# Kernel tuning notes

Hardware: AMD Instinct MI355X
Metric: run time of the kernel (lower is better)

## Reference

```python
import jax, jax.numpy as jnp
import numpy as np

KSIZE = 3
BJORCK_ITERS = 20
POWER_ITERS = 10


def _power_iteration_sigma(A, u):
    # A: [K, n, n], u: [K, n, 1] -> leading singular value per matrix, [K]
    for _ in range(POWER_ITERS):
        v = jnp.swapaxes(A, -1, -2) @ u
        v = v / jnp.linalg.norm(v, axis=-2, keepdims=True)
        u = A @ v
        u = u / jnp.linalg.norm(u, axis=-2, keepdims=True)
    s = (jnp.swapaxes(u, -1, -2) @ A @ v)[..., 0, 0]
    return s


def _bjorck(w, u):
    # power-iteration scaling is done under no_grad in torch -> stop_gradient
    s = jax.lax.stop_gradient(_power_iteration_sigma(jax.lax.stop_gradient(w), u))
    w = w / s[:, None, None]
    for _ in range(BJORCK_ITERS):
        wtw = jnp.swapaxes(w, -1, -2) @ w
        w = 1.5 * w - 0.5 * (w @ wtw)  # beta = 0.5, first order
    return w


def _block_orth(p1, p2):
    # -> [2, 2, n, n]
    n = p1.shape[0]
    I = jnp.eye(n, dtype=p1.dtype)
    return jnp.stack([
        jnp.stack([p1 @ p2, p1 @ (I - p2)]),
        jnp.stack([(I - p1) @ p2, (I - p1) @ (I - p2)]),
    ])


def _matrix_conv(m1, m2):
    # m1: [k,k,n,n], m2: [l,l,n,n] -> [k+l-1, k+l-1, n, n]
    k, l = m1.shape[0], m2.shape[0]
    size = k + l - 1
    rows = []
    for i in range(size):
        row = []
        for j in range(size):
            acc = 0.0
            for i1 in range(min(k, i + 1)):
                for j1 in range(min(k, j + 1)):
                    if i - i1 < l and j - j1 < l:
                        acc = acc + m1[i1, j1] @ m2[i - i1, j - j1]
            row.append(acc)
        rows.append(jnp.stack(row))
    return jnp.stack(rows)


def _bcop_weight(param_matrices, init_u):
    K, C, _ = param_matrices.shape  # K = 2*(KSIZE-1)+1, C = max_channels
    ortho = _bjorck(param_matrices, init_u)
    H = ortho[0]  # cin == cout == C, full slice
    half = C // 2
    mask = jnp.concatenate(
        [jnp.ones((K - 1, 1, half), ortho.dtype), jnp.zeros((K - 1, 1, C - half), ortho.dtype)],
        axis=-1)
    PQ = ortho[1:] * mask
    PQ = PQ @ jnp.swapaxes(PQ, -1, -2)  # symmetric projections [K-1, C, C]
    p = _block_orth(PQ[0], PQ[1])
    for t in range(1, KSIZE - 1):
        p = _matrix_conv(p, _block_orth(PQ[2 * t], PQ[2 * t + 1]))
    p = jnp.einsum('ab,ijbc->ijac', H, p)  # H @ p[i,j]
    # dict_to_tensor(...).permute(3, 2, 1, 0): [k, k, r, c] -> [c, r, j, i]
    return jnp.transpose(p, (3, 2, 1, 0))  # [C_out, C_in, KSIZE, KSIZE]


def setup_inputs() -> dict:
    key = jax.random.key(0)
    k1, k2, k3, k4 = jax.random.split(key, 4)
    C = 256
    num_kernels = 2 * (KSIZE - 1) + 1
    x = jax.random.normal(k1, (32, C, 64, 64), dtype=jnp.float32)
    param_matrices = jax.random.normal(k2, (num_kernels, C, C), dtype=jnp.float32) / np.sqrt(C)
    init_u = jax.random.normal(k3, (num_kernels, C, 1), dtype=jnp.float32)
    bias = jax.random.uniform(k4, (C,), dtype=jnp.float32, minval=-1.0 / np.sqrt(C), maxval=1.0 / np.sqrt(C))
    return {"x": x, "param_matrices": param_matrices, "init_u": init_u, "bias": bias}


def reference(x, param_matrices, init_u, bias):
    weight = _bcop_weight(param_matrices, init_u)
    # cyclic (circular) padding by k//2 on each side, odd kernel
    pad = KSIZE // 2
    xp = jnp.pad(x, ((0, 0), (0, 0), (pad, pad), (pad, pad)), mode='wrap')
    out = jax.lax.conv_general_dilated(
        xp, weight, window_strides=(1, 1), padding='VALID',
        dimension_numbers=('NCHW', 'OIHW', 'NCHW'))
    return out + bias[None, :, None, None]
```

## Files before the change

kernel.cpp:

```cpp
#include <hip/hip_runtime.h>
#include <stdint.h>

typedef unsigned short u16;
typedef unsigned short u16x4 __attribute__((ext_vector_type(4)));
typedef short bf16x8 __attribute__((ext_vector_type(8)));
typedef float f32x4 __attribute__((ext_vector_type(4)));

#define CDIM 256
#define MSZ 65536

constexpr size_t O_XB   = 0;
constexpr size_t O_AT   = 67108864;
constexpr size_t O_PQH  = 67108864;
constexpr size_t O_PQL  = O_PQH + 524288;
constexpr size_t O_SVAL = 68419584;
constexpr size_t O_W0   = 68419840;
constexpr size_t O_W1   = 71041280;
constexpr size_t O_PH   = 71041280;
constexpr size_t O_PL   = O_PH + 524288;
constexpr size_t O_QTH  = O_PL + 524288;
constexpr size_t O_QTL  = O_QTH + 524288;
constexpr size_t O_TH   = 73662720;
constexpr size_t O_TL   = O_TH + 655360;
constexpr size_t O_RTH  = 74973440;
constexpr size_t O_RTL  = O_RTH + 1179648;
constexpr size_t O_WBQ  = O_RTL + 1179648;

__device__ __forceinline__ u16 f2bf(float f) {
  union { float f; uint32_t u; } a; a.f = f;
  uint32_t u = a.u;
  uint32_t r = u + 0x7FFFu + ((u >> 16) & 1u);
  return (u16)(r >> 16);
}
__device__ __forceinline__ float bf2f(u16 u) {
  union { uint32_t u; float f; } a; a.u = ((uint32_t)u) << 16; return a.f;
}
__device__ __forceinline__ void split_st(u16* hi, u16* lo, float v) {
  u16 h = f2bf(v);
  *hi = h;
  *lo = f2bf(v - bf2f(h));
}
__device__ __forceinline__ void gl16(const void* g, void* l) {
  __builtin_amdgcn_global_load_lds(
      (const __attribute__((address_space(1))) void*)g,
      (__attribute__((address_space(3))) void*)l, 16, 0, 0);
}

__global__ void convert_k(const float* __restrict__ x, u16* __restrict__ xb) {
  __shared__ float t[32][33];
  int b = blockIdx.x;
  int ctile = b & 7, wtile = (b >> 3) & 1, h = (b >> 4) & 63, n = b >> 10;
  int c0 = ctile * 32, w0 = wtile * 32;
  int tid = threadIdx.x;
  for (int p = 0; p < 4; p++) {
    int e = tid + p * 256; int cc = e >> 5, ww = e & 31;
    t[cc][ww] = x[(((size_t)n * 256 + c0 + cc) * 64 + h) * 64 + w0 + ww];
  }
  __syncthreads();
  {
    int ww = tid >> 3, c4 = (tid & 7) * 4;
    u16x4 v;
    #pragma unroll
    for (int j = 0; j < 4; ++j) v[j] = f2bf(t[c4 + j][ww]);
    *(u16x4*)&xb[(((size_t)n * 64 + h) * 64 + w0 + ww) * 256 + c0 + c4] = v;
  }
}

__global__ void wtwA_k(const float* __restrict__ W, float* __restrict__ T) {
  int m = blockIdx.y;
  int i0 = (blockIdx.x >> 3) * 32, j0 = (blockIdx.x & 7) * 32;
  const float* A = W + (size_t)m * MSZ;
  __shared__ float As[32][33], Bs[32][33];
  int tid = threadIdx.x, tx = tid & 15, ty = tid >> 4;
  float a00 = 0, a01 = 0, a10 = 0, a11 = 0;
  for (int kc = 0; kc < CDIM; kc += 32) {
    __syncthreads();
    for (int p = 0; p < 4; p++) {
      int e = tid + p * 256; int kk = e >> 5, cc = e & 31;
      As[kk][cc] = A[(kc + kk) * CDIM + i0 + cc];
      Bs[kk][cc] = A[(kc + kk) * CDIM + j0 + cc];
    }
    __syncthreads();
    #pragma unroll
    for (int kk = 0; kk < 32; kk++) {
      float av0 = As[kk][ty], av1 = As[kk][ty + 16];
      float bv0 = Bs[kk][tx], bv1 = Bs[kk][tx + 16];
      a00 += av0 * bv0; a01 += av0 * bv1; a10 += av1 * bv0; a11 += av1 * bv1;
    }
  }
  float* Tm = T + (size_t)m * MSZ;
  Tm[(i0 + ty) * CDIM + j0 + tx] = a00;
  Tm[(i0 + ty) * CDIM + j0 + tx + 16] = a01;
  Tm[(i0 + ty + 16) * CDIM + j0 + tx] = a10;
  Tm[(i0 + ty + 16) * CDIM + j0 + tx + 16] = a11;
}

__global__ __launch_bounds__(1024) void powerB_k(const float* __restrict__ A,
                                                 const float* __restrict__ B,
                                                 const float* __restrict__ u0,
                                                 float* __restrict__ sval) {
  int m = blockIdx.x;
  int tid = threadIdx.x;
  int t = tid & 255, s = tid >> 8;
  __shared__ float v[256], part[4][257];
  const float* Am = A + (size_t)m * MSZ;
  const float* Bm = B + (size_t)m * MSZ;
  float a = 0.f;
  #pragma unroll 16
  for (int i = 0; i < 64; ++i) a += Am[(s * 64 + i) * 256 + t] * u0[m * 256 + s * 64 + i];
  part[s][t] = a;
  __syncthreads();
  if (s == 0) v[t] = part[0][t] + part[1][t] + part[2][t] + part[3][t];
  __syncthreads();
  for (int it = 0; it < 9; ++it) {
    float b = 0.f;
    #pragma unroll 16
    for (int j = 0; j < 64; ++j) b += Bm[(s * 64 + j) * 256 + t] * v[s * 64 + j];
    part[s][t] = b;
    __syncthreads();
    if (s == 0) v[t] = part[0][t] + part[1][t] + part[2][t] + part[3][t];
    __syncthreads();
  }
  float b = 0.f;
  #pragma unroll 16
  for (int j = 0; j < 64; ++j) b += Bm[(s * 64 + j) * 256 + t] * v[s * 64 + j];
  part[s][t] = b;
  __syncthreads();
  if (s == 0) {
    float w = part[0][t] + part[1][t] + part[2][t] + part[3][t];
    float vv = v[t];
    float d1 = vv * w, d2 = vv * vv;
    for (int off = 32; off; off >>= 1) {
      d1 += __shfl_down(d1, off);
      d2 += __shfl_down(d2, off);
    }
    if ((t & 63) == 0) { part[1][t >> 6] = d1; part[2][t >> 6] = d2; }
  }
  __syncthreads();
  if (tid == 0) {
    float num = part[1][0] + part[1][1] + part[1][2] + part[1][3];
    float den = part[2][0] + part[2][1] + part[2][2] + part[2][3];
    sval[m] = sqrtf(num / den);
  }
}

__global__ void scaleT_k(const float* __restrict__ param, const float* __restrict__ sval,
                         u16* __restrict__ Wh, u16* __restrict__ Wl,
                         u16* __restrict__ Wth, u16* __restrict__ Wtl) {
  __shared__ float tl[32][33];
  int m = blockIdx.y;
  int i0 = (blockIdx.x >> 3) * 32, j0 = (blockIdx.x & 7) * 32;
  int tid = threadIdx.x;
  float inv = 1.0f / sval[m];
  const float* Am = param + (size_t)m * MSZ;
  size_t mo = (size_t)m * MSZ;
  for (int p = 0; p < 4; ++p) {
    int e = tid + p * 256; int ii = e >> 5, jj = e & 31;
    float v = Am[(i0 + ii) * 256 + j0 + jj] * inv;
    tl[ii][jj] = v;
    size_t idx = mo + (size_t)(i0 + ii) * 256 + j0 + jj;
    split_st(&Wh[idx], &Wl[idx], v);
  }
  __syncthreads();
  for (int p = 0; p < 4; ++p) {
    int e = tid + p * 256; int jj = e >> 5, ii = e & 31;
    float v = tl[ii][jj];
    size_t idxT = mo + (size_t)(j0 + jj) * 256 + i0 + ii;
    split_st(&Wth[idxT], &Wtl[idxT], v);
  }
}

__device__ __forceinline__ void gemm32_acc(
    const u16* __restrict__ Ah, const u16* __restrict__ Al, int i0,
    const u16* __restrict__ Bh, const u16* __restrict__ Bl, int j0,
    int K, f32x4* acc, char* smem, int tid)
{
  int lane = tid & 63, wave = tid >> 6;
  int qm = wave >> 1, qn = wave & 1;
  int ra = qm * 16 + (lane & 15);
  int rb = qn * 16 + (lane & 15);
  int kb = (lane >> 4) * 16;
  for (int kc = 0; kc < K; kc += 128) {
    __syncthreads();
    #pragma unroll
    for (int p = 0; p < 8; ++p) {
      int e = tid + p * 256;
      int bufi = e >> 9;
      int r = (e >> 4) & 31;
      int cb = (e & 15) * 16;
      const u16* srcm = (bufi == 0) ? Ah : (bufi == 1) ? Al : (bufi == 2) ? Bh : Bl;
      int r0 = (bufi < 2) ? i0 : j0;
      const char* src = (const char*)srcm + ((size_t)(r0 + r) * 256 + kc) * 2 + cb;
      *(uint4*)(smem + bufi * 8192 + r * 256 + (cb ^ ((r & 7) << 4))) = *(const uint4*)src;
    }
    __syncthreads();
    #pragma unroll
    for (int ks = 0; ks < 4; ++ks) {
      int kbyte = ks * 64 + kb;
      int oa = ra * 256 + (kbyte ^ ((ra & 7) << 4));
      int ob = rb * 256 + (kbyte ^ ((rb & 7) << 4));
      bf16x8 ah = *(const bf16x8*)(smem + oa);
      bf16x8 al = *(const bf16x8*)(smem + 8192 + oa);
      bf16x8 bh = *(const bf16x8*)(smem + 16384 + ob);
      bf16x8 bl = *(const bf16x8*)(smem + 24576 + ob);
      *acc = __builtin_amdgcn_mfma_f32_16x16x32_bf16(ah, bh, *acc, 0, 0, 0);
      *acc = __builtin_amdgcn_mfma_f32_16x16x32_bf16(ah, bl, *acc, 0, 0, 0);
      *acc = __builtin_amdgcn_mfma_f32_16x16x32_bf16(al, bh, *acc, 0, 0, 0);
    }
  }
}

#define GEMM_IDX \
  int tid = threadIdx.x; \
  int lane = tid & 63, wave = tid >> 6, qm = wave >> 1, qn = wave & 1; \
  int orow = qm * 16 + ((lane >> 4) << 2); \
  int ocol = qn * 16 + (lane & 15); \
  int i0 = (blockIdx.x >> 3) * 32, j0 = (blockIdx.x & 7) * 32; \
  __shared__ char smem[32768];

__global__ __launch_bounds__(256) void bjorck_t_k(
    const u16* __restrict__ Wth, const u16* __restrict__ Wtl,
    u16* __restrict__ Th, u16* __restrict__ Tl) {
  GEMM_IDX
  size_t mo = (size_t)blockIdx.y * MSZ;
  f32x4 acc = {};
  gemm32_acc(Wth + mo, Wtl + mo, i0, Wth + mo, Wtl + mo, j0, 256, &acc, smem, tid);
  #pragma unroll
  for (int v = 0; v < 4; ++v) {
    size_t idx = mo + (size_t)(i0 + orow + v) * 256 + (j0 + ocol);
    split_st(&Th[idx], &Tl[idx], acc[v]);
  }
}

__global__ __launch_bounds__(256) void bjorck_u_k(
    const u16* __restrict__ Wh, const u16* __restrict__ Wl,
    const u16* __restrict__ Th, const u16* __restrict__ Tl,
    u16* __restrict__ nWh, u16* __restrict__ nWl,
    u16* __restrict__ nWth, u16* __restrict__ nWtl) {
  GEMM_IDX
  size_t mo = (size_t)blockIdx.y * MSZ;
  f32x4 acc = {};
  gemm32_acc(Wh + mo, Wl + mo, i0, Th + mo, Tl + mo, j0, 256, &acc, smem, tid);
  #pragma unroll
  for (int v = 0; v < 4; ++v) {
    int r = i0 + orow + v, c = j0 + ocol;
    size_t idx = mo + (size_t)r * 256 + c;
    float wv = bf2f(Wh[idx]) + bf2f(Wl[idx]);
    float nv = 1.5f * wv - 0.5f * acc[v];
    split_st(&nWh[idx], &nWl[idx], nv);
    size_t idxT = mo + (size_t)c * 256 + r;
    split_st(&nWth[idxT], &nWtl[idxT], nv);
  }
}

__global__ __launch_bounds__(256) void pq_k(
    const u16* __restrict__ Wh, const u16* __restrict__ Wl,
    u16* __restrict__ PQh, u16* __restrict__ PQl) {
  GEMM_IDX
  int m4 = blockIdx.y;
  const u16* Oh = Wh + (size_t)(1 + m4) * MSZ;
  const u16* Ol = Wl + (size_t)(1 + m4) * MSZ;
  f32x4 acc = {};
  gemm32_acc(Oh, Ol, i0, Oh, Ol, j0, 128, &acc, smem, tid);
  #pragma unroll
  for (int v = 0; v < 4; ++v) {
    size_t idx = (size_t)m4 * MSZ + (size_t)(i0 + orow + v) * 256 + (j0 + ocol);
    split_st(&PQh[idx], &PQl[idx], acc[v]);
  }
}

__global__ __launch_bounds__(256) void c12b_k(
    const u16* __restrict__ PQh, const u16* __restrict__ PQl,
    u16* __restrict__ Ph, u16* __restrict__ Pl,
    u16* __restrict__ QTh, u16* __restrict__ QTl) {
  GEMM_IDX
  f32x4 a1 = {}, a2t = {};
  gemm32_acc(PQh, PQl, i0, PQh + MSZ, PQl + MSZ, j0, 256, &a1, smem, tid);
  gemm32_acc(PQh + 3 * MSZ, PQl + 3 * MSZ, i0, PQh + 2 * MSZ, PQl + 2 * MSZ, j0,
             256, &a2t, smem, tid);
  #pragma unroll
  for (int v = 0; v < 4; ++v) {
    int row = i0 + orow + v, col = j0 + ocol;
    size_t g = (size_t)row * 256 + col;
    float I = (row == col) ? 1.f : 0.f;
    float p0 = bf2f(PQh[g]) + bf2f(PQl[g]);
    float p1 = bf2f(PQh[MSZ + g]) + bf2f(PQl[MSZ + g]);
    float c1 = a1[v];
    split_st(&Ph[g],           &Pl[g],           c1);
    split_st(&Ph[MSZ + g],     &Pl[MSZ + g],     p0 - c1);
    split_st(&Ph[2*MSZ + g],   &Pl[2*MSZ + g],   p1 - c1);
    split_st(&Ph[3*MSZ + g],   &Pl[3*MSZ + g],   I - p0 - p1 + c1);
    float q0 = bf2f(PQh[2*MSZ + g]) + bf2f(PQl[2*MSZ + g]);
    float q1 = bf2f(PQh[3*MSZ + g]) + bf2f(PQl[3*MSZ + g]);
    float c2t = a2t[v];
    split_st(&QTh[g],          &QTl[g],          c2t);
    split_st(&QTh[MSZ + g],    &QTl[MSZ + g],    q0 - c2t);
    split_st(&QTh[2*MSZ + g],  &QTl[2*MSZ + g],  q1 - c2t);
    split_st(&QTh[3*MSZ + g],  &QTl[3*MSZ + g],  I - q0 - q1 + c2t);
  }
}

__global__ __launch_bounds__(256) void mconv_k(
    const u16* __restrict__ Ph, const u16* __restrict__ Pl,
    const u16* __restrict__ QTh, const u16* __restrict__ QTl,
    u16* __restrict__ RTh, u16* __restrict__ RTl) {
  GEMM_IDX
  int ij = blockIdx.y;
  const int toff[10] = {0, 1, 3, 4, 6, 10, 12, 13, 15, 16};
  const int tp[16] = {0, 0, 1, 1, 0, 2, 0, 1, 2, 3, 1, 3, 2, 2, 3, 3};
  const int tq[16] = {0, 1, 0, 1, 2, 0, 3, 2, 1, 0, 3, 1, 2, 3, 2, 3};
  f32x4 acc = {};
  for (int t = toff[ij]; t < toff[ij + 1]; ++t) {
    gemm32_acc(Ph + (size_t)tp[t] * MSZ, Pl + (size_t)tp[t] * MSZ, i0,
               QTh + (size_t)tq[t] * MSZ, QTl + (size_t)tq[t] * MSZ, j0, 256, &acc, smem, tid);
  }
  #pragma unroll
  for (int v = 0; v < 4; ++v) {
    int r = i0 + orow + v, c = j0 + ocol;
    size_t idxT = (size_t)ij * MSZ + (size_t)c * 256 + r;
    split_st(&RTh[idxT], &RTl[idxT], acc[v]);
  }
}

__global__ __launch_bounds__(256) void final_k(
    const u16* __restrict__ Hh, const u16* __restrict__ Hl,
    const u16* __restrict__ RTh, const u16* __restrict__ RTl,
    u16* __restrict__ WBQ) {
  GEMM_IDX
  int ij = blockIdx.y;
  f32x4 acc = {};
  gemm32_acc(Hh, Hl, i0, RTh + (size_t)ij * MSZ, RTl + (size_t)ij * MSZ, j0,
             256, &acc, smem, tid);
  #pragma unroll
  for (int v = 0; v < 4; ++v) {
    int r = i0 + orow + v, c = j0 + ocol;
    int ct = r >> 6, ks = (r >> 5) & 1, jj = (r >> 3) & 3, e = r & 7;
    int s = jj ^ (c & 3);
    int g = ct * 18 + ij * 2 + ks;
    WBQ[(size_t)g * 8192 + (size_t)(c * 4 + s) * 8 + e] = f2bf(acc[v]);
  }
}

__global__ __launch_bounds__(512, 2) void conv_k(
    const u16* __restrict__ xb, const u16* __restrict__ Wb,
    const float* __restrict__ bias, float* __restrict__ out) {
  int braw = blockIdx.x;
  int L = (braw & 7) * 128 + (braw >> 3);
  int h2 = L & 31, n = L >> 5;
  int h0 = h2 * 2;
  int tid = threadIdx.x;
  int lane = tid & 63, wave = tid >> 6;
  int wm = wave >> 2, wn = wave & 3;
  int fr = lane & 15, q = lane >> 4;

  __shared__ char smem[65536];
  char* sX = smem;
  char* sW = smem + 32768;

  f32x4 acc[4][4] = {};

  auto issueX = [&](int ct) {
    #pragma unroll
    for (int i = 0; i < 4; ++i) {
      int d = (wave * 4 + i) * 64 + lane;
      int cb = (d & 7) * 16;
      int w = (d >> 3) & 63;
      int r = d >> 9;
      int hs = (h0 - 1 + r) & 63;
      const char* src = (const char*)xb + (((size_t)(n * 64 + hs) * 64 + w) << 9)
                        + ct * 128 + (cb ^ ((w & 7) << 4));
      gl16(src, sX + (wave * 4 + i) * 1024);
    }
  };
  auto issueW = [&](int g) {
    const char* base = (const char*)Wb + (size_t)g * 16384;
    char* dst = sW + (g & 1) * 16384;
    #pragma unroll
    for (int i = 0; i < 2; ++i) {
      int c = (wave * 2 + i) * 64 + lane;
      gl16(base + c * 16, dst + (wave * 2 + i) * 1024);
    }
  };

  issueX(0);
  issueW(0);
  __syncthreads();

  for (int g = 0; g < 72; ++g) {
    int ct = g / 18, r18 = g % 18, tap = r18 >> 1, ks = r18 & 1;
    int kh = tap % 3, kw = tap / 3;
    if (g + 1 < 72) issueW(g + 1);
    const char* wb = sW + (g & 1) * 16384;
    __builtin_amdgcn_s_setprio(1);
    {
      bf16x8 af[4], bfr[4];
      #pragma unroll
      for (int fn = 0; fn < 4; ++fn) {
        int cl = wn * 64 + fn * 16 + fr;
        bfr[fn] = *(const bf16x8*)(wb + cl * 64 + ((q * 16) ^ ((cl & 3) << 4)));
      }
      int kb2 = ks * 64 + q * 16;
      #pragma unroll
      for (int fm = 0; fm < 4; ++fm) {
        int wsrc = (fm * 16 + fr + kw + 63) & 63;
        af[fm] = *(const bf16x8*)(sX + ((wm + kh) * 64 + wsrc) * 128 + (kb2 ^ ((wsrc & 7) << 4)));
      }
      #pragma unroll
      for (int fm = 0; fm < 4; ++fm)
        #pragma unroll
        for (int fn = 0; fn < 4; ++fn)
          acc[fm][fn] = __builtin_amdgcn_mfma_f32_16x16x32_bf16(af[fm], bfr[fn], acc[fm][fn], 0, 0, 0);
    }
    __builtin_amdgcn_s_setprio(0);
    if (r18 == 17 && ct < 3) {
      __syncthreads();
      issueX(ct + 1);
      __syncthreads();
    } else {
      __syncthreads();
    }
  }

  __syncthreads();
  float* sF = (float*)smem;
  #pragma unroll
  for (int r = 0; r < 2; ++r) {
    if ((wn >> 1) == r) {
      #pragma unroll
      for (int fn = 0; fn < 4; ++fn) {
        int cl = (wn & 1) * 64 + fn * 16 + fr;
        float bv = bias[r * 128 + cl];
        #pragma unroll
        for (int fm = 0; fm < 4; ++fm) {
          f32x4 v = acc[fm][fn];
          v[0] += bv; v[1] += bv; v[2] += bv; v[3] += bv;
          *(f32x4*)((char*)sF + cl * 512 + wm * 256 +
                    (((unsigned)(fm * 64 + q * 16)) ^ ((unsigned)(cl & 7) << 4))) = v;
        }
      }
    }
    __syncthreads();
    #pragma unroll
    for (int p = 0; p < 8; ++p) {
      int e = tid + p * 512;
      int w4 = e & 15, hloc = (e >> 4) & 1, cl = e >> 5;
      f32x4 val = *(const f32x4*)((const char*)sF + cl * 512 + hloc * 256 +
                                  (((unsigned)(w4 * 16)) ^ ((unsigned)(cl & 7) << 4)));
      *(f32x4*)(out + (((size_t)n * 256 + r * 128 + cl) * 64 + (h0 + hloc)) * 64 + w4 * 4) = val;
    }
    if (r == 0) __syncthreads();
  }
}

extern "C" void kernel_launch(void* const* d_in, const int* in_sizes, int n_in,
                              void* d_out, int out_size, void* d_ws, size_t ws_size,
                              hipStream_t stream) {
  const float* x = (const float*)d_in[0];
  const float* param = (const float*)d_in[1];
  const float* u0 = (const float*)d_in[2];
  const float* bias = (const float*)d_in[3];
  float* out = (float*)d_out;
  char* ws = (char*)d_ws;
  (void)in_sizes; (void)n_in; (void)out_size; (void)ws_size;

  float* B = (float*)(ws + O_AT);
  float* sval = (float*)(ws + O_SVAL);
  u16* W0h  = (u16*)(ws + O_W0);   u16* W0l  = W0h + 327680;
  u16* W0th = W0l + 327680;        u16* W0tl = W0th + 327680;
  u16* W1h  = (u16*)(ws + O_W1);   u16* W1l  = W1h + 327680;
  u16* W1th = W1l + 327680;        u16* W1tl = W1th + 327680;
  u16* Th = (u16*)(ws + O_TH);     u16* Tl = (u16*)(ws + O_TL);
  u16* PQh = (u16*)(ws + O_PQH);   u16* PQl = (u16*)(ws + O_PQL);
  u16* Ph = (u16*)(ws + O_PH);     u16* Pl = (u16*)(ws + O_PL);
  u16* QTh = (u16*)(ws + O_QTH);   u16* QTl = (u16*)(ws + O_QTL);
  u16* RTh = (u16*)(ws + O_RTH);   u16* RTl = (u16*)(ws + O_RTL);
  u16* WBQ = (u16*)(ws + O_WBQ);

  convert_k<<<32768, 256, 0, stream>>>(x, (u16*)(ws + O_XB));
  wtwA_k<<<dim3(64, 5), 256, 0, stream>>>(param, B);
  powerB_k<<<5, 1024, 0, stream>>>(param, B, u0, sval);
  scaleT_k<<<dim3(64, 5), 256, 0, stream>>>(param, sval, W0h, W0l, W0th, W0tl);

  u16 *cWh = W0h, *cWl = W0l, *cWth = W0th, *cWtl = W0tl;
  u16 *nWh = W1h, *nWl = W1l, *nWth = W1th, *nWtl = W1tl;
  for (int it = 0; it < 20; ++it) {
    bjorck_t_k<<<dim3(64, 5), 256, 0, stream>>>(cWth, cWtl, Th, Tl);
    bjorck_u_k<<<dim3(64, 5), 256, 0, stream>>>(cWh, cWl, Th, Tl, nWh, nWl, nWth, nWtl);
    u16* t0;
    t0 = cWh; cWh = nWh; nWh = t0;
    t0 = cWl; cWl = nWl; nWl = t0;
    t0 = cWth; cWth = nWth; nWth = t0;
    t0 = cWtl; cWtl = nWtl; nWtl = t0;
  }

  pq_k<<<dim3(64, 4), 256, 0, stream>>>(cWh, cWl, PQh, PQl);
  c12b_k<<<64, 256, 0, stream>>>(PQh, PQl, Ph, Pl, QTh, QTl);
  mconv_k<<<dim3(64, 9), 256, 0, stream>>>(Ph, Pl, QTh, QTl, RTh, RTl);
  final_k<<<dim3(64, 9), 256, 0, stream>>>(cWh, cWl, RTh, RTl, WBQ);

  conv_k<<<1024, 512, 0, stream>>>((const u16*)(ws + O_XB), WBQ, bias, out);
}
```

Measured before the change: 488.0 us.

## Fuse Bjorck WtW and update GEMMs into one column-strip kernel

```diff
diff --git a/kernel.cpp b/kernel.cpp
--- a/kernel.cpp
+++ b/kernel.cpp
@@ -20,8 +20,6 @@
 constexpr size_t O_PL   = O_PH + 524288;
 constexpr size_t O_QTH  = O_PL + 524288;
 constexpr size_t O_QTL  = O_QTH + 524288;
-constexpr size_t O_TH   = 73662720;
-constexpr size_t O_TL   = O_TH + 655360;
 constexpr size_t O_RTH  = 74973440;
 constexpr size_t O_RTL  = O_RTH + 1179648;
 constexpr size_t O_WBQ  = O_RTL + 1179648;
@@ -218,38 +216,98 @@
   int i0 = (blockIdx.x >> 3) * 32, j0 = (blockIdx.x & 7) * 32; \
   __shared__ char smem[32768];
 
-__global__ __launch_bounds__(256) void bjorck_t_k(
+__global__ __launch_bounds__(256, 1) void bjorck_f_k(
+    const u16* __restrict__ Wh, const u16* __restrict__ Wl,
     const u16* __restrict__ Wth, const u16* __restrict__ Wtl,
-    u16* __restrict__ Th, u16* __restrict__ Tl) {
-  GEMM_IDX
-  size_t mo = (size_t)blockIdx.y * MSZ;
-  f32x4 acc = {};
-  gemm32_acc(Wth + mo, Wtl + mo, i0, Wth + mo, Wtl + mo, j0, 256, &acc, smem, tid);
-  #pragma unroll
-  for (int v = 0; v < 4; ++v) {
-    size_t idx = mo + (size_t)(i0 + orow + v) * 256 + (j0 + ocol);
-    split_st(&Th[idx], &Tl[idx], acc[v]);
-  }
-}
-
-__global__ __launch_bounds__(256) void bjorck_u_k(
-    const u16* __restrict__ Wh, const u16* __restrict__ Wl,
-    const u16* __restrict__ Th, const u16* __restrict__ Tl,
     u16* __restrict__ nWh, u16* __restrict__ nWl,
     u16* __restrict__ nWth, u16* __restrict__ nWtl) {
-  GEMM_IDX
-  size_t mo = (size_t)blockIdx.y * MSZ;
-  f32x4 acc = {};
-  gemm32_acc(Wh + mo, Wl + mo, i0, Th + mo, Tl + mo, j0, 256, &acc, smem, tid);
-  #pragma unroll
-  for (int v = 0; v < 4; ++v) {
-    int r = i0 + orow + v, c = j0 + ocol;
-    size_t idx = mo + (size_t)r * 256 + c;
-    float wv = bf2f(Wh[idx]) + bf2f(Wl[idx]);
-    float nv = 1.5f * wv - 0.5f * acc[v];
-    split_st(&nWh[idx], &nWl[idx], nv);
-    size_t idxT = mo + (size_t)c * 256 + r;
-    split_st(&nWth[idxT], &nWtl[idxT], nv);
+  __shared__ char smem[131072];
+  char* sB = smem;
+  char* sT = smem + 32768;
+  char* sA = smem + 65536;
+  int tid = threadIdx.x;
+  int lane = tid & 63, wave = tid >> 6;
+  int qm = wave >> 1, qn = wave & 1;
+  int fr = lane & 15, q = lane >> 4;
+  int m = blockIdx.y, jp = blockIdx.x;
+  int j0 = jp * 32;
+  size_t mo = (size_t)m * MSZ;
+
+  auto stageH = [&](const u16* src, int r0, char* dst) {
+    #pragma unroll
+    for (int p = 0; p < 4; ++p) {
+      int c = tid + p * 256;
+      int r = c >> 5;
+      int cb = ((c & 31) * 16) ^ ((r & 7) << 4);
+      gl16((const char*)src + (size_t)(r0 + r) * 512 + cb,
+           dst + p * 4096 + wave * 1024);
+    }
+  };
+  auto stageA = [&](int buf, const u16* mh, const u16* ml, int i) {
+    stageH(mh + mo, i * 32, sA + buf * 32768);
+    stageH(ml + mo, i * 32, sA + buf * 32768 + 16384);
+  };
+  int ra = qm * 16 + fr;
+  int rb = qn * 16 + fr;
+  auto tile = [&](const char* abase, const char* bbase) -> f32x4 {
+    f32x4 acc = {};
+    #pragma unroll
+    for (int ks = 0; ks < 8; ++ks) {
+      int kb = ks * 64 + q * 16;
+      int oa = ra * 512 + (kb ^ ((ra & 7) << 4));
+      int ob = rb * 512 + (kb ^ ((rb & 7) << 4));
+      bf16x8 ah = *(const bf16x8*)(abase + oa);
+      bf16x8 al = *(const bf16x8*)(abase + 16384 + oa);
+      bf16x8 bh = *(const bf16x8*)(bbase + ob);
+      bf16x8 bl = *(const bf16x8*)(bbase + 16384 + ob);
+      acc = __builtin_amdgcn_mfma_f32_16x16x32_bf16(ah, bh, acc, 0, 0, 0);
+      acc = __builtin_amdgcn_mfma_f32_16x16x32_bf16(ah, bl, acc, 0, 0, 0);
+      acc = __builtin_amdgcn_mfma_f32_16x16x32_bf16(al, bh, acc, 0, 0, 0);
+    }
+    return acc;
+  };
+
+  stageH(Wth + mo, j0, sB);
+  stageH(Wtl + mo, j0, sB + 16384);
+  stageA(0, Wth, Wtl, 0);
+  __syncthreads();
+
+  int buf = 0;
+  for (int i = 0; i < 8; ++i) {
+    if (i < 7) stageA(buf ^ 1, Wth, Wtl, i + 1);
+    else       stageA(buf ^ 1, Wh, Wl, 0);
+    f32x4 acc = tile(sA + buf * 32768, sB);
+    int i0 = i * 32;
+    int k0 = i0 + qm * 16 + q * 4;
+    int ocol = qn * 16 + fr;
+    u16x4 h4, l4;
+    #pragma unroll
+    for (int v = 0; v < 4; ++v) {
+      u16 h = f2bf(acc[v]);
+      h4[v] = h; l4[v] = f2bf(acc[v] - bf2f(h));
+    }
+    unsigned boff = (unsigned)(ocol * 512) + (((unsigned)(k0 * 2)) ^ ((unsigned)(ocol & 7) << 4));
+    *(u16x4*)(sT + boff) = h4;
+    *(u16x4*)(sT + 16384 + boff) = l4;
+    __syncthreads();
+    buf ^= 1;
+  }
+  for (int i = 0; i < 8; ++i) {
+    if (i < 7) stageA(buf ^ 1, Wh, Wl, i + 1);
+    f32x4 acc = tile(sA + buf * 32768, sT);
+    int i0 = i * 32;
+    #pragma unroll
+    for (int v = 0; v < 4; ++v) {
+      int r = i0 + qm * 16 + q * 4 + v, c = j0 + qn * 16 + fr;
+      size_t idx = mo + (size_t)r * 256 + c;
+      float wv = bf2f(Wh[idx]) + bf2f(Wl[idx]);
+      float nv = 1.5f * wv - 0.5f * acc[v];
+      split_st(&nWh[idx], &nWl[idx], nv);
+      size_t idxT = mo + (size_t)c * 256 + r;
+      split_st(&nWth[idxT], &nWtl[idxT], nv);
+    }
+    __syncthreads();
+    buf ^= 1;
   }
 }
 
@@ -372,9 +430,9 @@
       gl16(src, sX + (wave * 4 + i) * 1024);
     }
   };
-  auto issueW = [&](int g) {
+  auto issueW = [&](int g, int par) {
     const char* base = (const char*)Wb + (size_t)g * 16384;
-    char* dst = sW + (g & 1) * 16384;
+    char* dst = sW + par * 16384;
     #pragma unroll
     for (int i = 0; i < 2; ++i) {
       int c = (wave * 2 + i) * 64 + lane;
@@ -383,41 +441,50 @@
   };
 
   issueX(0);
-  issueW(0);
-  __syncthreads();
-
-  for (int g = 0; g < 72; ++g) {
-    int ct = g / 18, r18 = g % 18, tap = r18 >> 1, ks = r18 & 1;
-    int kh = tap % 3, kw = tap / 3;
-    if (g + 1 < 72) issueW(g + 1);
-    const char* wb = sW + (g & 1) * 16384;
-    __builtin_amdgcn_s_setprio(1);
-    {
-      bf16x8 af[4], bfr[4];
-      #pragma unroll
-      for (int fn = 0; fn < 4; ++fn) {
-        int cl = wn * 64 + fn * 16 + fr;
-        bfr[fn] = *(const bf16x8*)(wb + cl * 64 + ((q * 16) ^ ((cl & 3) << 4)));
+  issueW(0, 0);
+  __syncthreads();
+
+  for (int ct = 0; ct < 4; ++ct) {
+    #pragma unroll
+    for (int r18 = 0; r18 < 18; ++r18) {
+      const int tap = r18 >> 1, ks = r18 & 1;
+      const int kh = tap % 3, kw = tap / 3;
+      if (r18 < 17) issueW(ct * 18 + r18 + 1, (r18 + 1) & 1);
+      else if (ct < 3) issueW((ct + 1) * 18, 0);
+      const char* wb = sW + (r18 & 1) * 16384;
+      __builtin_amdgcn_s_setprio(1);
+      {
+        bf16x8 af[4], bfr[4];
+        #pragma unroll
+        for (int fn = 0; fn < 4; ++fn) {
+          int cl = wn * 64 + fn * 16 + fr;
+          bfr[fn] = *(const bf16x8*)(wb + cl * 64 + ((q * 16) ^ ((cl & 3) << 4)));
+        }
+        const int kbase = ks * 64;
+        #pragma unroll
+        for (int fm = 0; fm < 4; ++fm) {
+          int wsrc = (fm * 16 + fr + kw + 63) & 63;
+          af[fm] = *(const bf16x8*)(sX + ((wm + kh) * 64 + wsrc) * 128 +
+                                    ((kbase + q * 16) ^ ((wsrc & 7) << 4)));
+        }
+        #pragma unroll
+        for (int fm = 0; fm < 4; ++fm)
+          #pragma unroll
+          for (int fn = 0; fn < 4; ++fn)
+            acc[fm][fn] = __builtin_amdgcn_mfma_f32_16x16x32_bf16(af[fm], bfr[fn], acc[fm][fn], 0, 0, 0);
       }
-      int kb2 = ks * 64 + q * 16;
-      #pragma unroll
-      for (int fm = 0; fm < 4; ++fm) {
-        int wsrc = (fm * 16 + fr + kw + 63) & 63;
-        af[fm] = *(const bf16x8*)(sX + ((wm + kh) * 64 + wsrc) * 128 + (kb2 ^ ((wsrc & 7) << 4)));
+      __builtin_amdgcn_s_setprio(0);
+      if (r18 == 17) {
+        if (ct < 3) {
+          __syncthreads();
+          issueX(ct + 1);
+          __syncthreads();
+        } else {
+          __syncthreads();
+        }
+      } else {
+        __syncthreads();
       }
-      #pragma unroll
-      for (int fm = 0; fm < 4; ++fm)
-        #pragma unroll
-        for (int fn = 0; fn < 4; ++fn)
-          acc[fm][fn] = __builtin_amdgcn_mfma_f32_16x16x32_bf16(af[fm], bfr[fn], acc[fm][fn], 0, 0, 0);
-    }
-    __builtin_amdgcn_s_setprio(0);
-    if (r18 == 17 && ct < 3) {
-      __syncthreads();
-      issueX(ct + 1);
-      __syncthreads();
-    } else {
-      __syncthreads();
     }
   }
 
@@ -469,7 +536,6 @@
   u16* W0th = W0l + 327680;        u16* W0tl = W0th + 327680;
   u16* W1h  = (u16*)(ws + O_W1);   u16* W1l  = W1h + 327680;
   u16* W1th = W1l + 327680;        u16* W1tl = W1th + 327680;
-  u16* Th = (u16*)(ws + O_TH);     u16* Tl = (u16*)(ws + O_TL);
   u16* PQh = (u16*)(ws + O_PQH);   u16* PQl = (u16*)(ws + O_PQL);
   u16* Ph = (u16*)(ws + O_PH);     u16* Pl = (u16*)(ws + O_PL);
   u16* QTh = (u16*)(ws + O_QTH);   u16* QTl = (u16*)(ws + O_QTL);
@@ -484,8 +550,8 @@
   u16 *cWh = W0h, *cWl = W0l, *cWth = W0th, *cWtl = W0tl;
   u16 *nWh = W1h, *nWl = W1l, *nWth = W1th, *nWtl = W1tl;
   for (int it = 0; it < 20; ++it) {
-    bjorck_t_k<<<dim3(64, 5), 256, 0, stream>>>(cWth, cWtl, Th, Tl);
-    bjorck_u_k<<<dim3(64, 5), 256, 0, stream>>>(cWh, cWl, Th, Tl, nWh, nWl, nWth, nWtl);
+    bjorck_f_k<<<dim3(8, 5), 256, 0, stream>>>(cWh, cWl, cWth, cWtl,
+                                               nWh, nWl, nWth, nWtl);
     u16* t0;
     t0 = cWh; cWh = nWh; nWh = t0;
     t0 = cWl; cWl = nWl; nWl = t0;
```

New measurement: 653.5 us. +33.9%, slower.
